# Performance work log

Measured on AMD Instinct MI355X. Metric: run time of the kernel, lower is better.

Reference implementation:

```python
import jax, jax.numpy as jnp
import numpy as np

B, T, S = 4, 4096, 4096
D_MODEL = 512        # d_query = d_value_in = d_key_in
N_HEADS = 8
D_KEY = 512
D_VALUE = 512
N_OMEGA = 64
EPS = 1e-9
DK_H = D_KEY // N_HEADS      # 64
DV_H = D_VALUE // N_HEADS    # 64


def _glorot(key, shape):
    fan_in, fan_out = shape[-2], shape[-1]
    lim = np.sqrt(6.0 / (fan_in + fan_out))
    return jax.random.uniform(key, shape, jnp.float32, -lim, lim)


def _draw_omega(key, d_feature, n_omega):
    # n_omega == d_feature here -> single orthogonal block scaled by sqrt(d)
    g = jax.random.normal(key, (d_feature, d_feature), jnp.float32)
    q, _ = jnp.linalg.qr(g)
    q = q * jnp.sqrt(jnp.float32(d_feature))
    return q[:n_omega]


def setup_inputs() -> dict:
    key = jax.random.key(0)
    ks = jax.random.split(key, 7)
    return {
        "query": 0.5 * jax.random.normal(ks[0], (B, T, D_MODEL), jnp.float32),
        "value": 0.5 * jax.random.normal(ks[1], (B, S, D_MODEL), jnp.float32),
        "key": 0.5 * jax.random.normal(ks[2], (B, S, D_MODEL), jnp.float32),
        "wq": _glorot(ks[3], (N_HEADS, D_MODEL, DK_H)),
        "wv": _glorot(ks[4], (N_HEADS, D_MODEL, DV_H)),
        "wk": _glorot(ks[5], (N_HEADS, D_MODEL, DK_H)),
        "omega": _draw_omega(ks[6], DK_H, N_OMEGA),
    }


def _phi(x, omega):
    # x: (B,H,T,dk_h) -> (B,H,T,2*n_omega) FAVOR+ positive random features
    square_sum = 0.5 * jnp.sum(x * x, axis=-1, keepdims=True)
    xw = jnp.einsum('bhtk,mk->bhtm', x, omega)
    un = jnp.exp(jnp.concatenate([xw, -xw], axis=-1) - square_sum) + EPS
    return un / jnp.sqrt(jnp.float32(2.0 * N_OMEGA))


def reference(query, value, key, wq, wv, wk, omega):
    q = jnp.einsum('btf,hfk->bhtk', query, wq)   # (B,H,T,dk_h)
    v = jnp.einsum('bsd,hdk->bhsk', value, wv)   # (B,H,S,dv_h)
    k = jnp.einsum('bsf,hfk->bhsk', key, wk)     # (B,H,S,dk_h)
    qp = _phi(q, omega)                          # (B,H,T,2M)
    kp = _phi(k, omega)                          # (B,H,S,2M)
    v1 = jnp.concatenate([v, jnp.ones(v.shape[:-1] + (1,), v.dtype)], axis=-1)
    kv = jnp.einsum('bhsm,bhsd->bhmd', kp, v1)   # (B,H,2M,dv_h+1)
    qkv = jnp.einsum('bhtm,bhmd->bhtd', qp, kv)  # (B,H,T,dv_h+1)
    normalizer = qkv[..., -1:]
    out = qkv[..., :-1] / normalizer
    # faithful to original: plain reshape (B,H,T,dv_h) -> (B,T,D_VALUE), no transpose
    return jnp.reshape(out, (B, T, D_VALUE))
```

## Files before the change

### kernel.cpp

```cpp
#include <hip/hip_runtime.h>

typedef _Float16 half8 __attribute__((ext_vector_type(8)));
typedef _Float16 half4_t __attribute__((ext_vector_type(4)));
typedef short short8 __attribute__((ext_vector_type(8)));
typedef unsigned short u16x4 __attribute__((ext_vector_type(4)));
typedef float f32x4 __attribute__((ext_vector_type(4)));

#define NH 8

__device__ __forceinline__ unsigned short f2bf(float x) {
  union { float f; unsigned u; } v; v.f = x;
  unsigned r = v.u + 0x7FFFu + ((v.u >> 16) & 1u);
  return (unsigned short)(r >> 16);
}

#define DRAIN_BAR()                                  \
  asm volatile("s_waitcnt lgkmcnt(0)" ::: "memory"); \
  __builtin_amdgcn_s_barrier();                      \
  __builtin_amdgcn_sched_barrier(0)

#define WAITVM(N) asm volatile("s_waitcnt vmcnt(" #N ")" ::: "memory")

#define GLOAD_LDS16(g, l)                                             \
  __builtin_amdgcn_global_load_lds(                                   \
      (const __attribute__((address_space(1))) unsigned int*)(g),     \
      (__attribute__((address_space(3))) unsigned int*)(l), 16, 0, 0)

__global__ __launch_bounds__(256) void k0_qk(
    const float* __restrict__ wq, const float* __restrict__ wk,
    const float* __restrict__ omega,
    _Float16* __restrict__ wxq, _Float16* __restrict__ wxk) {
  const int bid = blockIdx.x;
  const int arr = bid >> 7;
  const int h = (bid >> 4) & 7;
  const int ft = (bid >> 1) & 7;
  const int os = bid & 1;
  const int f = threadIdx.x & 63;
  const int w = threadIdx.x >> 6;
  const float* wsrc = (arr ? wk : wq) + ((size_t)h * 512 + ft * 64 + f) * 64;
  float wreg[64];
#pragma unroll
  for (int i = 0; i < 16; ++i) {
    float4 v = *(const float4*)(wsrc + i * 4);
    wreg[i * 4] = v.x; wreg[i * 4 + 1] = v.y; wreg[i * 4 + 2] = v.z; wreg[i * 4 + 3] = v.w;
  }
  _Float16* outp = arr ? wxk : wxq;
  const int k8 = f >> 3, e = f & 7;
#pragma unroll 1
  for (int oo = 0; oo < 8; ++oo) {
    const int o = w * 16 + os * 8 + oo;
    const float* om = omega + o * 64;
    float s = 0.f;
#pragma unroll
    for (int k = 0; k < 64; ++k) s = fmaf(wreg[k], om[k], s);
    outp[((((size_t)h * 8 + ft) * 8 + k8) * 64 + o) * 8 + e] = (_Float16)s;
  }
}

__global__ __launch_bounds__(256) void k0_v(
    const float* __restrict__ wv, _Float16* __restrict__ wvt) {
  int idx = blockIdx.x * 256 + threadIdx.x;
  int h = idx >> 15, o = (idx >> 9) & 63, f = idx & 511;
  float val = wv[((size_t)h * 512 + f) * 64 + o];
  wvt[((((size_t)h * 8 + (f >> 6)) * 8 + ((f >> 3) & 7)) * 64 + o) * 8 + (f & 7)] = (_Float16)val;
}

__global__ __launch_bounds__(512, 1) void fused_kv(
    const float* __restrict__ key, const float* __restrict__ value,
    const _Float16* __restrict__ wxk, const _Float16* __restrict__ wvt,
    float* __restrict__ kvpart) {
  __shared__ __align__(16) _Float16 A[2][128][72];
  __shared__ __align__(16) _Float16 W[2][2][4096];
  __shared__ __align__(16) unsigned short kpT[128][136];
  __shared__ __align__(16) unsigned short vT[64][136];
  const int bid = blockIdx.x;
  const int hp = bid >> 6;
  const int b = (bid >> 4) & 3;
  const int sc = bid & 15;
  const int s0 = sc * 256;
  const int tid = threadIdx.x;
  const int w = tid >> 6;
  const int lane = tid & 63;
  const int g = lane >> 4, c = lane & 15;
  const int hh = w >> 2;
  const int rq = w & 3;
  const int xr = lane >> 4;
  const int xc = (lane & 15) * 4;

  const _Float16* wkb0 = wxk + (size_t)(hp * 2) * 32768;
  const _Float16* wkb1 = wkb0 + 32768;
  const _Float16* wvb0 = wvt + (size_t)(hp * 2) * 32768;
  const _Float16* wvb1 = wvb0 + 32768;

  short8 bones;
#pragma unroll
  for (int i = 0; i < 8; ++i) bones[i] = (c == 0) ? (short)0x3F80 : (short)0;

  f32x4 acc_kv[2][5];
#pragma unroll
  for (int h2 = 0; h2 < 2; ++h2)
#pragma unroll
    for (int j = 0; j < 5; ++j) acc_kv[h2][j] = (f32x4){0.f, 0.f, 0.f, 0.f};

  u16x4 kps[2][4], kms[2][4], vs_[2][4];

  float4 xv[4];
  half8 wr0, wr1;

#pragma unroll 1
  for (int p = 0; p < 4; ++p) {
    const float* xb = ((p & 1) ? value : key) +
                      (size_t)(b * 4096 + s0 + (p >> 1) * 128 + w * 16 + xr) * 512 + xc;
    const _Float16* wb0 = (p & 1) ? wvb0 : wkb0;
    const _Float16* wb1 = (p & 1) ? wvb1 : wkb1;

#pragma unroll
    for (int i = 0; i < 4; ++i) xv[i] = *(const float4*)(xb + i * 2048);
    wr0 = *(const half8*)(wb0 + tid * 8);
    wr1 = *(const half8*)(wb1 + tid * 8);
#pragma unroll
    for (int i = 0; i < 4; ++i) {
      float vv[4] = {xv[i].x, xv[i].y, xv[i].z, xv[i].w};
      half4_t hv;
#pragma unroll
      for (int j2 = 0; j2 < 4; ++j2) hv[j2] = (_Float16)vv[j2];
      *(half4_t*)&A[0][w * 16 + i * 4 + xr][xc] = hv;
    }
    *(half8*)&W[0][0][tid * 8] = wr0;
    *(half8*)&W[0][1][tid * 8] = wr1;
#pragma unroll
    for (int i = 0; i < 4; ++i) xv[i] = *(const float4*)(xb + 64 + i * 2048);
    wr0 = *(const half8*)(wb0 + 4096 + tid * 8);
    wr1 = *(const half8*)(wb1 + 4096 + tid * 8);
    DRAIN_BAR();

    f32x4 accp[2][4];
#pragma unroll
    for (int mf = 0; mf < 2; ++mf)
#pragma unroll
      for (int j = 0; j < 4; ++j) accp[mf][j] = (f32x4){0.f, 0.f, 0.f, 0.f};

#pragma unroll 1
    for (int kc = 0; kc < 8; ++kc) {
      const int cur = kc & 1;
      if (kc < 7) {
        const int nxt = cur ^ 1;
#pragma unroll
        for (int i = 0; i < 4; ++i) {
          float vv[4] = {xv[i].x, xv[i].y, xv[i].z, xv[i].w};
          half4_t hv;
#pragma unroll
          for (int j2 = 0; j2 < 4; ++j2) hv[j2] = (_Float16)vv[j2];
          *(half4_t*)&A[nxt][w * 16 + i * 4 + xr][xc] = hv;
        }
        *(half8*)&W[nxt][0][tid * 8] = wr0;
        *(half8*)&W[nxt][1][tid * 8] = wr1;
        if (kc < 6) {
#pragma unroll
          for (int i = 0; i < 4; ++i)
            xv[i] = *(const float4*)(xb + (kc + 2) * 64 + i * 2048);
          wr0 = *(const half8*)(wb0 + (kc + 2) * 4096 + tid * 8);
          wr1 = *(const half8*)(wb1 + (kc + 2) * 4096 + tid * 8);
        }
      }
#pragma unroll
      for (int ks = 0; ks < 2; ++ks) {
        half8 af0 = *(const half8*)&A[cur][rq * 32 + c][ks * 32 + g * 8];
        half8 af1 = *(const half8*)&A[cur][rq * 32 + 16 + c][ks * 32 + g * 8];
#pragma unroll
        for (int nf = 0; nf < 4; ++nf) {
          half8 wf = *(const half8*)&W[cur][hh][((ks * 4 + g) * 64 + nf * 16 + c) * 8];
          accp[0][nf] = __builtin_amdgcn_mfma_f32_16x16x32_f16(af0, wf, accp[0][nf], 0, 0, 0);
          accp[1][nf] = __builtin_amdgcn_mfma_f32_16x16x32_f16(af1, wf, accp[1][nf], 0, 0, 0);
        }
      }
      DRAIN_BAR();
    }

    if ((p & 1) == 0) {
#pragma unroll
      for (int mf = 0; mf < 2; ++mf) {
        float ss_[4];
#pragma unroll
        for (int j = 0; j < 4; ++j) {
          float s = 0.f;
#pragma unroll
          for (int nf = 0; nf < 4; ++nf) { float q = accp[mf][nf][j]; s = fmaf(q, q, s); }
          s += __shfl_xor(s, 1); s += __shfl_xor(s, 2);
          s += __shfl_xor(s, 4); s += __shfl_xor(s, 8);
          ss_[j] = s * 0.0078125f;
        }
#pragma unroll
        for (int nf = 0; nf < 4; ++nf) {
          u16x4 kp_p, kp_m;
#pragma unroll
          for (int j = 0; j < 4; ++j) {
            float v = accp[mf][nf][j];
            kp_p[j] = f2bf(__expf(v - ss_[j]) + 1e-9f);
            kp_m[j] = f2bf(__expf(-v - ss_[j]) + 1e-9f);
          }
          kps[mf][nf] = kp_p;
          kms[mf][nf] = kp_m;
        }
      }
    } else {
#pragma unroll
      for (int mf = 0; mf < 2; ++mf)
#pragma unroll
        for (int nf = 0; nf < 4; ++nf) {
          u16x4 vv;
#pragma unroll
          for (int j = 0; j < 4; ++j) vv[j] = f2bf(accp[mf][nf][j]);
          vs_[mf][nf] = vv;
        }
#pragma unroll
      for (int h2 = 0; h2 < 2; ++h2) {
        if (hh == h2) {
#pragma unroll
          for (int mf = 0; mf < 2; ++mf)
#pragma unroll
            for (int nf = 0; nf < 4; ++nf) {
              const int m = nf * 16 + c;
              const int sl = rq * 32 + mf * 16 + g * 4;
              *(u16x4*)&kpT[m][sl] = kps[mf][nf];
              *(u16x4*)&kpT[64 + m][sl] = kms[mf][nf];
              *(u16x4*)&vT[m][sl] = vs_[mf][nf];
            }
        }
        DRAIN_BAR();
#pragma unroll
        for (int ks = 0; ks < 4; ++ks) {
          short8 a = *(const short8*)&kpT[w * 16 + c][ks * 32 + g * 8];
#pragma unroll
          for (int nf = 0; nf < 4; ++nf) {
            short8 bb = *(const short8*)&vT[nf * 16 + c][ks * 32 + g * 8];
            acc_kv[h2][nf] = __builtin_amdgcn_mfma_f32_16x16x32_bf16(a, bb, acc_kv[h2][nf], 0, 0, 0);
          }
          acc_kv[h2][4] = __builtin_amdgcn_mfma_f32_16x16x32_bf16(a, bones, acc_kv[h2][4], 0, 0, 0);
        }
        __builtin_amdgcn_s_barrier();
      }
    }
  }

#pragma unroll
  for (int h2 = 0; h2 < 2; ++h2) {
    float* pbase = kvpart + ((size_t)sc * 32 + b * 8 + hp * 2 + h2) * 10240;
#pragma unroll
    for (int nf = 0; nf < 5; ++nf)
#pragma unroll
      for (int j = 0; j < 4; ++j)
        pbase[(w * 16 + g * 4 + j) * 80 + nf * 16 + c] = acc_kv[h2][nf][j];
  }
}

__global__ __launch_bounds__(128) void k3a_denom(
    const float* __restrict__ kvpart, float* __restrict__ invbuf,
    float* __restrict__ lsc) {
  const int bh = blockIdx.x;
  const int m = threadIdx.x;
  const float* base = kvpart + (size_t)bh * 10240 + m * 80 + 64;
  float s = 0.f;
#pragma unroll
  for (int kk = 0; kk < 16; ++kk) s += base[(size_t)kk * 327680];
  invbuf[bh * 128 + m] = 1.0f / s;
  lsc[bh * 128 + m] = __logf(s);
}

__global__ __launch_bounds__(256) void k3b_reduce(
    const float* __restrict__ kvpart, const float* __restrict__ invbuf,
    _Float16* __restrict__ kvnt) {
  const int bh = blockIdx.x;
  const int e0 = blockIdx.y * 1024 + threadIdx.x * 4;
  const int m = e0 / 80;
  const int d0 = e0 - m * 80;
  const float* base = kvpart + (size_t)bh * 10240 + e0;
  f32x4 s = (f32x4){0.f, 0.f, 0.f, 0.f};
#pragma unroll
  for (int kk = 0; kk < 16; ++kk) {
    f32x4 v = *(const f32x4*)(base + (size_t)kk * 327680);
    s += v;
  }
  const float inv = invbuf[bh * 128 + m];
  const int mst = ((m & 63) << 1) | (m >> 6);
  _Float16* outb = kvnt + (size_t)bh * 10240 + mst;
#pragma unroll
  for (int j = 0; j < 4; ++j) {
    const int d = d0 + j;
    float val;
    if (d < 64) val = s[j] * inv;
    else if (d == 64) val = 1.0f;
    else val = 0.f;
    outb[d * 128] = (_Float16)val;
  }
}

__global__ __launch_bounds__(256, 3) void fused_qo(
    const float* __restrict__ query, const _Float16* __restrict__ wxq,
    const _Float16* __restrict__ kvnt, const float* __restrict__ lsc,
    float* __restrict__ out) {
  __shared__ __align__(16) _Float16 A_[64][136];
  __shared__ __align__(16) _Float16 W4[4][4096];
  const int bid = blockIdx.x;
  const int hh2 = bid >> 8;
  const int b = (bid >> 6) & 3;
  const int tt = bid & 63;
  const int t0 = tt * 64;
  const int tid = threadIdx.x;
  const int w = tid >> 6;
  const int lane = tid & 63;
  const int g = lane >> 4, c = lane & 15;
  const int arow = tid >> 2;
  const int acb = (tid & 3) * 32;

  const float* xq = query + (size_t)(b * 4096 + t0 + arow) * 512 + acb;
  const char* wbase = (const char*)wxq;

  f32x4 accp[4][4];
#pragma unroll
  for (int h = 0; h < 4; ++h)
#pragma unroll
    for (int j = 0; j < 4; ++j) accp[h][j] = (f32x4){0.f, 0.f, 0.f, 0.f};

  float4 xv[8];

#define ISSUE_W(S)                                                              \
  do {                                                                          \
    const int kq_ = (S) >> 3, loc_ = (S) & 7, h_ = loc_ >> 1, kc2_ = loc_ & 1;  \
    const size_t woff = (((size_t)(hh2 * 4 + h_) * 8 + kq_ * 2 + kc2_) * 4096) * 2; \
    const char* gb = wbase + woff + (w * 2) * 1024 + lane * 16;                 \
    char* lb = (char*)&W4[(S) & 3][0] + (w * 2) * 1024;                         \
    GLOAD_LDS16(gb, lb);                                                        \
    GLOAD_LDS16(gb + 1024, lb + 1024);                                          \
  } while (0)

#pragma unroll
  for (int i = 0; i < 8; ++i) xv[i] = *(const float4*)(xq + i * 4);
  ISSUE_W(0);
  ISSUE_W(1);
  ISSUE_W(2);

#pragma unroll
  for (int kq = 0; kq < 4; ++kq) {
    if (kq > 0) { DRAIN_BAR(); }
#pragma unroll
    for (int i = 0; i < 8; i += 2) {
      half8 hv;
      hv[0] = (_Float16)xv[i].x;     hv[1] = (_Float16)xv[i].y;
      hv[2] = (_Float16)xv[i].z;     hv[3] = (_Float16)xv[i].w;
      hv[4] = (_Float16)xv[i + 1].x; hv[5] = (_Float16)xv[i + 1].y;
      hv[6] = (_Float16)xv[i + 1].z; hv[7] = (_Float16)xv[i + 1].w;
      *(half8*)&A_[arow][acb + i * 4] = hv;
    }
    DRAIN_BAR();

#pragma unroll
    for (int loc = 0; loc < 8; ++loc) {
      const int S = kq * 8 + loc;
      if (S == 31)      { WAITVM(0); }
      else if (S == 30) { WAITVM(2); }
      else if (loc >= 6){ WAITVM(12); }
      else              { WAITVM(4); }
      __builtin_amdgcn_s_barrier();
      __builtin_amdgcn_sched_barrier(0);
      if (S + 3 < 32) ISSUE_W(S + 3);
      if (loc == 5 && kq < 3) {
#pragma unroll
        for (int i = 0; i < 8; ++i)
          xv[i] = *(const float4*)(xq + (kq + 1) * 128 + i * 4);
      }
      const int h = loc >> 1;
      const int kc2 = loc & 1;
      const int buf = S & 3;
#pragma unroll
      for (int ks = 0; ks < 2; ++ks) {
        half8 a = *(const half8*)&A_[w * 16 + c][kc2 * 64 + ks * 32 + g * 8];
#pragma unroll
        for (int nf = 0; nf < 4; ++nf) {
          half8 wf = *(const half8*)&W4[buf][((ks * 4 + g) * 64 + nf * 16 + c) * 8];
          accp[h][nf] = __builtin_amdgcn_mfma_f32_16x16x32_f16(a, wf, accp[h][nf], 0, 0, 0);
        }
      }
    }
  }
#undef ISSUE_W

  DRAIN_BAR();

#pragma unroll
  for (int h = 0; h < 4; ++h) {
    const int bh = b * NH + hh2 * 4 + h;
    float Lp[4], Lm[4];
#pragma unroll
    for (int nf = 0; nf < 4; ++nf) {
      Lp[nf] = lsc[bh * 128 + nf * 16 + c];
      Lm[nf] = lsc[bh * 128 + 64 + nf * 16 + c];
    }
    float ss_[4], cm_[4];
#pragma unroll
    for (int j = 0; j < 4; ++j) {
      float s = 0.f;
#pragma unroll
      for (int nf = 0; nf < 4; ++nf) { float q = accp[h][nf][j]; s = fmaf(q, q, s); }
      s += __shfl_xor(s, 1); s += __shfl_xor(s, 2);
      s += __shfl_xor(s, 4); s += __shfl_xor(s, 8);
      ss_[j] = s * 0.0078125f;
    }
#pragma unroll
    for (int j = 0; j < 4; ++j) {
      float m0 = -1e30f;
#pragma unroll
      for (int nf = 0; nf < 4; ++nf) {
        float v = accp[h][nf][j];
        m0 = fmaxf(m0, fmaxf(v - ss_[j] + Lp[nf], -v - ss_[j] + Lm[nf]));
        m0 = fmaxf(m0, fmaxf(Lp[nf], Lm[nf]) - 20.723265f);
      }
      m0 = fmaxf(m0, __shfl_xor(m0, 1)); m0 = fmaxf(m0, __shfl_xor(m0, 2));
      m0 = fmaxf(m0, __shfl_xor(m0, 4)); m0 = fmaxf(m0, __shfl_xor(m0, 8));
      cm_[j] = m0;
    }
#pragma unroll
    for (int nf = 0; nf < 4; ++nf) {
      const int m = nf * 16 + c;
#pragma unroll
      for (int j = 0; j < 4; ++j) {
        float v = accp[h][nf][j];
        _Float16 pp = (_Float16)(__expf(v - ss_[j] + Lp[nf] - cm_[j]) +
                                 1e-9f * __expf(Lp[nf] - cm_[j]));
        _Float16 pm = (_Float16)(__expf(-v - ss_[j] + Lm[nf] - cm_[j]) +
                                 1e-9f * __expf(Lm[nf] - cm_[j]));
        union { unsigned u; _Float16 hh_[2]; } pk;
        pk.hh_[0] = pp; pk.hh_[1] = pm;
        *(unsigned*)&A_[w * 16 + g * 4 + j][2 * m] = pk.u;
      }
    }
    DRAIN_BAR();

    f32x4 acco[5];
#pragma unroll
    for (int j = 0; j < 5; ++j) acco[j] = (f32x4){0.f, 0.f, 0.f, 0.f};
    const _Float16* kvb = kvnt + (size_t)bh * 10240;
#pragma unroll
    for (int ks = 0; ks < 4; ++ks) {
      half8 a = *(const half8*)&A_[w * 16 + c][ks * 32 + g * 8];
#pragma unroll
      for (int nf = 0; nf < 5; ++nf) {
        half8 bb = *(const half8*)(kvb + (size_t)(nf * 16 + c) * 128 + ks * 32 + g * 8);
        acco[nf] = __builtin_amdgcn_mfma_f32_16x16x32_f16(a, bb, acco[nf], 0, 0, 0);
      }
    }
    const int tb = t0 + w * 16 + g * 4;
#pragma unroll
    for (int j = 0; j < 4; ++j) {
      float nrm = __shfl(acco[4][j], (lane & 48));
      float invn = 1.0f / nrm;
#pragma unroll
      for (int nf = 0; nf < 4; ++nf) {
        out[((size_t)bh * 4096 + tb + j) * 64 + nf * 16 + c] = acco[nf][j] * invn;
      }
    }
    DRAIN_BAR();
  }
}

extern "C" void kernel_launch(void* const* d_in, const int* in_sizes, int n_in,
                              void* d_out, int out_size, void* d_ws, size_t ws_size,
                              hipStream_t stream) {
  const float* query = (const float*)d_in[0];
  const float* value = (const float*)d_in[1];
  const float* key   = (const float*)d_in[2];
  const float* wq    = (const float*)d_in[3];
  const float* wv    = (const float*)d_in[4];
  const float* wk    = (const float*)d_in[5];
  const float* omega = (const float*)d_in[6];
  float* out = (float*)d_out;
  char* ws = (char*)d_ws;

  _Float16* wxq  = (_Float16*)(ws);
  _Float16* wxk  = (_Float16*)(ws + 524288);
  _Float16* wvt  = (_Float16*)(ws + 1048576);
  float* kvpart  = (float*)(ws + 1572864);
  _Float16* kvnt = (_Float16*)(ws + 22544384);
  float* lsc     = (float*)(ws + 23199744);
  float* invbuf  = (float*)(ws + 23216128);

  k0_qk<<<256, 256, 0, stream>>>(wq, wk, omega, wxq, wxk);
  k0_v<<<1024, 256, 0, stream>>>(wv, wvt);
  fused_kv<<<256, 512, 0, stream>>>(key, value, wxk, wvt, kvpart);
  k3a_denom<<<32, 128, 0, stream>>>(kvpart, invbuf, lsc);
  k3b_reduce<<<dim3(32, 10), 256, 0, stream>>>(kvpart, invbuf, kvnt);
  fused_qo<<<512, 256, 0, stream>>>(query, wxq, kvnt, lsc, out);
}
```

Measured before the change: 113.9 us.

## Load projection weights directly into registers instead of LDS staging in fused_qo

Replaces the async global-to-LDS 4-stage weight pipeline with a 3-deep register ring of half8 fragments loaded directly from global memory, removing per-step barriers and LDS traffic for weights. It also moves the next query chunk prefetch earlier and relaxes launch bounds from 3 to 2 blocks per SM to fit the larger register footprint. Each wave now reads the weights independently, so the same data is fetched redundantly across the four waves. Lower occupancy may hurt latency hiding.

Result: slower. 117.8 us (+3.4%).

```diff
diff --git a/kernel.cpp b/kernel.cpp
--- a/kernel.cpp
+++ b/kernel.cpp
@@ -18,13 +18,6 @@
   asm volatile("s_waitcnt lgkmcnt(0)" ::: "memory"); \
   __builtin_amdgcn_s_barrier();                      \
   __builtin_amdgcn_sched_barrier(0)
-
-#define WAITVM(N) asm volatile("s_waitcnt vmcnt(" #N ")" ::: "memory")
-
-#define GLOAD_LDS16(g, l)                                             \
-  __builtin_amdgcn_global_load_lds(                                   \
-      (const __attribute__((address_space(1))) unsigned int*)(g),     \
-      (__attribute__((address_space(3))) unsigned int*)(l), 16, 0, 0)
 
 __global__ __launch_bounds__(256) void k0_qk(
     const float* __restrict__ wq, const float* __restrict__ wk,
@@ -295,12 +288,11 @@
   }
 }
 
-__global__ __launch_bounds__(256, 3) void fused_qo(
+__global__ __launch_bounds__(256, 2) void fused_qo(
     const float* __restrict__ query, const _Float16* __restrict__ wxq,
     const _Float16* __restrict__ kvnt, const float* __restrict__ lsc,
     float* __restrict__ out) {
   __shared__ __align__(16) _Float16 A_[64][136];
-  __shared__ __align__(16) _Float16 W4[4][4096];
   const int bid = blockIdx.x;
   const int hh2 = bid >> 8;
   const int b = (bid >> 6) & 3;
@@ -314,7 +306,6 @@
   const int acb = (tid & 3) * 32;
 
   const float* xq = query + (size_t)(b * 4096 + t0 + arow) * 512 + acb;
-  const char* wbase = (const char*)wxq;
 
   f32x4 accp[4][4];
 #pragma unroll
@@ -323,22 +314,25 @@
     for (int j = 0; j < 4; ++j) accp[h][j] = (f32x4){0.f, 0.f, 0.f, 0.f};
 
   float4 xv[8];
-
-#define ISSUE_W(S)                                                              \
-  do {                                                                          \
-    const int kq_ = (S) >> 3, loc_ = (S) & 7, h_ = loc_ >> 1, kc2_ = loc_ & 1;  \
-    const size_t woff = (((size_t)(hh2 * 4 + h_) * 8 + kq_ * 2 + kc2_) * 4096) * 2; \
-    const char* gb = wbase + woff + (w * 2) * 1024 + lane * 16;                 \
-    char* lb = (char*)&W4[(S) & 3][0] + (w * 2) * 1024;                         \
-    GLOAD_LDS16(gb, lb);                                                        \
-    GLOAD_LDS16(gb + 1024, lb + 1024);                                          \
+  half8 wregs[3][8];
+
+#define ISSUE_WREG(S)                                                         \
+  do {                                                                        \
+    const int kq_ = (S) >> 3, loc_ = (S) & 7, h_ = loc_ >> 1, kc2_ = loc_ & 1;\
+    const _Float16* ws =                                                      \
+        wxq + ((size_t)(hh2 * 4 + h_) * 8 + kq_ * 2 + kc2_) * 4096;           \
+    _Pragma("unroll")                                                         \
+    for (int r = 0; r < 8; ++r) {                                             \
+      const int ks_ = r >> 2, nf_ = r & 3;                                    \
+      wregs[(S) % 3][r] =                                                     \
+          *(const half8*)(ws + (((ks_ * 4 + g) * 64) + nf_ * 16 + c) * 8);    \
+    }                                                                         \
   } while (0)
 
 #pragma unroll
   for (int i = 0; i < 8; ++i) xv[i] = *(const float4*)(xq + i * 4);
-  ISSUE_W(0);
-  ISSUE_W(1);
-  ISSUE_W(2);
+  ISSUE_WREG(0);
+  ISSUE_WREG(1);
 
 #pragma unroll
   for (int kq = 0; kq < 4; ++kq) {
@@ -352,38 +346,31 @@
       hv[6] = (_Float16)xv[i + 1].z; hv[7] = (_Float16)xv[i + 1].w;
       *(half8*)&A_[arow][acb + i * 4] = hv;
     }
+    if (kq < 3) {
+#pragma unroll
+      for (int i = 0; i < 8; ++i)
+        xv[i] = *(const float4*)(xq + (kq + 1) * 128 + i * 4);
+    }
     DRAIN_BAR();
 
 #pragma unroll
     for (int loc = 0; loc < 8; ++loc) {
       const int S = kq * 8 + loc;
-      if (S == 31)      { WAITVM(0); }
-      else if (S == 30) { WAITVM(2); }
-      else if (loc >= 6){ WAITVM(12); }
-      else              { WAITVM(4); }
-      __builtin_amdgcn_s_barrier();
-      __builtin_amdgcn_sched_barrier(0);
-      if (S + 3 < 32) ISSUE_W(S + 3);
-      if (loc == 5 && kq < 3) {
-#pragma unroll
-        for (int i = 0; i < 8; ++i)
-          xv[i] = *(const float4*)(xq + (kq + 1) * 128 + i * 4);
-      }
+      if (S + 2 < 32) ISSUE_WREG(S + 2);
       const int h = loc >> 1;
       const int kc2 = loc & 1;
-      const int buf = S & 3;
 #pragma unroll
       for (int ks = 0; ks < 2; ++ks) {
         half8 a = *(const half8*)&A_[w * 16 + c][kc2 * 64 + ks * 32 + g * 8];
 #pragma unroll
         for (int nf = 0; nf < 4; ++nf) {
-          half8 wf = *(const half8*)&W4[buf][((ks * 4 + g) * 64 + nf * 16 + c) * 8];
-          accp[h][nf] = __builtin_amdgcn_mfma_f32_16x16x32_f16(a, wf, accp[h][nf], 0, 0, 0);
-        }
-      }
-    }
-  }
-#undef ISSUE_W
+          accp[h][nf] = __builtin_amdgcn_mfma_f32_16x16x32_f16(
+              a, wregs[S % 3][ks * 4 + nf], accp[h][nf], 0, 0, 0);
+        }
+      }
+    }
+  }
+#undef ISSUE_WREG
 
   DRAIN_BAR();
 
```
